# Performance work log

Measured on AMD Instinct MI355X. Metric: run time of the kernel, lower is better.

Reference implementation:

```python
import jax, jax.numpy as jnp
import numpy as np

COLOR_SIZE = 4
SIZE = 64
FILTERS = 512
LENGTH = SIZE * SIZE * 3  # 12288


def setup_inputs() -> dict:
    key = jax.random.key(0)
    k1, k2, k3 = jax.random.split(key, 3)
    example = jax.random.randint(k1, (8, SIZE, SIZE, 3), 0, COLOR_SIZE, dtype=jnp.int32)
    kernel = jax.random.normal(k2, (FILTERS, LENGTH), dtype=jnp.float32)
    bias = jnp.zeros((FILTERS,), dtype=jnp.float32)
    dense_w = jax.random.normal(k3, (FILTERS, COLOR_SIZE), dtype=jnp.float32) * 0.02
    dense_b = jnp.zeros((COLOR_SIZE,), dtype=jnp.float32)
    return {"example": example, "kernel": kernel, "bias": bias,
            "dense_w": dense_w, "dense_b": dense_b}


def reference(example, kernel, bias, dense_w, dense_b):
    B = example.shape[0]
    L = kernel.shape[1]  # 12288
    # normalize int pixels to [-1, 1)
    x = example.astype(jnp.float32) / COLOR_SIZE * 2.0 - 1.0
    x = x.reshape(B, L)                                   # [B, L]
    # FFT-based long (causal full) convolution, fft_length = 2L
    Xf = jnp.fft.rfft(x, n=2 * L, axis=-1)                # [B, L+1] complex64
    Kf = jnp.fft.rfft(kernel, n=2 * L, axis=-1)           # [F, L+1]
    y = jnp.fft.irfft(Xf[:, None, :] * Kf[None, :, :], n=2 * L, axis=-1)[..., :L]  # [B, F, L]
    y = jnp.transpose(y, (0, 2, 1)) + bias                # [B, L, F]
    y = jax.nn.relu(y)
    out = y @ dense_w + dense_b                           # [B, L, color_size]
    return out.reshape(B, SIZE, SIZE, 3, COLOR_SIZE).astype(jnp.float32)
```

## Files before the change

kernel.cpp:

```cpp
#include <hip/hip_runtime.h>

#define FF 512
#define LL 12288
#define NJC 1556
#define NR 128

typedef _Float16 half8 __attribute__((ext_vector_type(8)));
typedef float    f32x16 __attribute__((ext_vector_type(16)));

__global__ __launch_bounds__(256) void build_At(const float* __restrict__ kern,
                                                _Float16* __restrict__ At) {
    int tid  = blockIdx.x * 256 + threadIdx.x;
    int lane = tid & 63;
    int rest = tid >> 6;
    int kc   = rest % 768;
    int fgt  = rest / 768;
    int f    = fgt * 32 + (lane & 31);
    int d0   = kc * 16 + (lane >> 5) * 8;
    const float* src = kern + (size_t)f * LL + d0;
    half8 v;
#pragma unroll
    for (int i = 0; i < 8; ++i) v[i] = (_Float16)src[i];
    ((half8*)At)[tid] = v;
}

__global__ __launch_bounds__(256) void build_XB(const int* __restrict__ ex,
                                                _Float16* __restrict__ XB) {
    int tid = blockIdx.x * 256 + threadIdx.x;
    if (tid >= NJC * NR) return;
    int r  = tid & 127;
    int jc = tid >> 7;
    int s  = r >> 3, b = r & 7;
    int j0 = jc * 8;
    half8 v;
#pragma unroll
    for (int i = 0; i < 8; ++i) {
        int idx = LL - 1 - (j0 + i) - s;
        float x = 0.f;
        if (idx >= 0) x = (float)ex[b * LL + idx] * 0.5f - 1.0f;
        v[i] = (_Float16)x;
    }
    ((half8*)XB)[tid] = v;
}

__global__ __launch_bounds__(256) void init_out(const float* __restrict__ db,
                                                float* __restrict__ out) {
    int tid = blockIdx.x * 256 + threadIdx.x;
    out[tid] = db[tid & 3];
}

__device__ __forceinline__ void gl_lds16(const half8* g, half8* l) {
    __builtin_amdgcn_global_load_lds((const __attribute__((address_space(1))) void*)g,
                                     (__attribute__((address_space(3))) void*)l, 16, 0, 0);
}

__global__ __launch_bounds__(256, 2) void conv_main(const _Float16* __restrict__ At,
                                                    const _Float16* __restrict__ XB,
                                                    const float* __restrict__ bias,
                                                    const float* __restrict__ dw,
                                                    float* __restrict__ out) {
    __shared__ half8 Abuf[2][8][4][64];

    int bx    = blockIdx.x;
    int slot  = bx & 7;
    int f_blk = slot >> 1;
    int n_blk = 383 - ((bx >> 3) * 2 + (slot & 1));
    int n0 = n_blk << 5;
    int M  = (n_blk + 4) >> 2;

    int tid  = threadIdx.x;
    int lane = tid & 63;
    int wid  = tid >> 6;
    int bb   = lane & 7;
    int nq   = (lane >> 3) & 3;
    int kh   = lane >> 5;

    const half8* Ag = (const half8*)At;
    const half8* ag[8];
#pragma unroll
    for (int u = 0; u < 8; ++u) {
        int kcl = wid * 2 + (u >> 2);
        int ft  = u & 3;
        ag[u] = Ag + ((size_t)(f_blk * 4 + ft) * 768 + kcl) * 64 + lane;
    }

    const half8* Bg = (const half8*)XB;
    const half8* pB[2];
#pragma unroll
    for (int cf = 0; cf < 2; ++cf) {
        int n  = n0 + wid * 8 + cf * 4 + nq;
        int T  = LL - 1 - n + 8 * kh;
        pB[cf] = Bg + (size_t)(T >> 3) * 128 + (T & 7) * 8 + bb;
    }

    f32x16 acc[4][2];
#pragma unroll
    for (int rf = 0; rf < 4; ++rf)
#pragma unroll
        for (int cf = 0; cf < 2; ++cf)
#pragma unroll
            for (int i = 0; i < 16; ++i) acc[rf][cf][i] = 0.f;

#pragma unroll
    for (int u = 0; u < 8; ++u)
        gl_lds16(ag[u], &Abuf[0][wid * 2 + (u >> 2)][u & 3][lane]);
    half8 b0[2], b1[2], b2[2];
#pragma unroll
    for (int cf = 0; cf < 2; ++cf) {
        b0[cf] = pB[cf][0];
        b1[cf] = pB[cf][256];
        pB[cf] += 512;
    }
    __syncthreads();

    for (int mc = 0; mc < M; ++mc) {
        int buf = mc & 1;
        if (mc + 1 < M) {
            size_t oa = (size_t)(mc + 1) * 512;
#pragma unroll
            for (int u = 0; u < 8; ++u)
                gl_lds16(ag[u] + oa, &Abuf[buf ^ 1][wid * 2 + (u >> 2)][u & 3][lane]);
        }
#pragma unroll
        for (int kc = 0; kc < 8; ++kc) {
#pragma unroll
            for (int cf = 0; cf < 2; ++cf) { b2[cf] = pB[cf][0]; pB[cf] += 256; }
            half8 a[4];
#pragma unroll
            for (int rf = 0; rf < 4; ++rf) a[rf] = Abuf[buf][kc][rf][lane];
#pragma unroll
            for (int rf = 0; rf < 4; ++rf)
#pragma unroll
                for (int cf = 0; cf < 2; ++cf)
                    acc[rf][cf] = __builtin_amdgcn_mfma_f32_32x32x16_f16(a[rf], b0[cf], acc[rf][cf], 0, 0, 0);
#pragma unroll
            for (int cf = 0; cf < 2; ++cf) { b0[cf] = b1[cf]; b1[cf] = b2[cf]; }
        }
        __syncthreads();
    }

    float p[2][4];
#pragma unroll
    for (int cf = 0; cf < 2; ++cf)
#pragma unroll
        for (int c = 0; c < 4; ++c) p[cf][c] = 0.f;

#pragma unroll
    for (int rf = 0; rf < 4; ++rf) {
#pragma unroll
        for (int reg = 0; reg < 16; ++reg) {
            int f = f_blk * 128 + rf * 32 + (reg & 3) + 8 * (reg >> 2) + 4 * kh;
            float bs = bias[f];
            float4 w = *(const float4*)(dw + (size_t)f * 4);
#pragma unroll
            for (int cf = 0; cf < 2; ++cf) {
                float y = fmaxf(acc[rf][cf][reg] + bs, 0.f);
                p[cf][0] += y * w.x; p[cf][1] += y * w.y;
                p[cf][2] += y * w.z; p[cf][3] += y * w.w;
            }
        }
    }
#pragma unroll
    for (int cf = 0; cf < 2; ++cf)
#pragma unroll
        for (int c = 0; c < 4; ++c)
            p[cf][c] += __shfl_xor(p[cf][c], 32, 64);
    if (kh == 0) {
#pragma unroll
        for (int cf = 0; cf < 2; ++cf) {
            int n = n0 + wid * 8 + cf * 4 + nq;
            float* o = out + ((size_t)bb * LL + n) * 4;
#pragma unroll
            for (int c = 0; c < 4; ++c) atomicAdd(o + c, p[cf][c]);
        }
    }
}

extern "C" void kernel_launch(void* const* d_in, const int* in_sizes, int n_in,
                              void* d_out, int out_size, void* d_ws, size_t ws_size,
                              hipStream_t stream) {
    const int*   ex   = (const int*)d_in[0];
    const float* kern = (const float*)d_in[1];
    const float* bias = (const float*)d_in[2];
    const float* dw   = (const float*)d_in[3];
    const float* db   = (const float*)d_in[4];
    float* out = (float*)d_out;

    _Float16* At = (_Float16*)d_ws;
    _Float16* XB = (_Float16*)((char*)d_ws + (size_t)FF * LL * 2);

    hipLaunchKernelGGL(build_At, dim3(3072), dim3(256), 0, stream, kern, At);
    hipLaunchKernelGGL(build_XB, dim3(778),  dim3(256), 0, stream, ex, XB);
    hipLaunchKernelGGL(init_out, dim3(1536), dim3(256), 0, stream, db, out);
    hipLaunchKernelGGL(conv_main, dim3(1536), dim3(256), 0, stream, At, XB, bias, dw, out);
}
```

Measured before the change: 534.5 us.

## Replace syncthreads with vmcnt-limited barriers and deepen B-operand prefetch

Replaces each __syncthreads in the main GEMM loop with an explicit s_waitcnt vmcnt plus s_barrier. The wait drains only the older LDS-bound A loads and leaves the newer B register loads in flight across the barrier. The kc loop now processes two k-chunks per step, with B operands prefetched a full step ahead, and raises wave priority around the MFMA bursts. The guard on the next-chunk prefetch is removed, so the last iteration issues an extra A prefetch. For the final filter tile that prefetch reads past the At region into the adjacent workspace and writes into an unused LDS buffer. The hand-written wait counts rely on exact load ordering, which is fragile.

Measured after the change: 565.1 us. 5.7% more time.

```diff
diff --git a/kernel.cpp b/kernel.cpp
--- a/kernel.cpp
+++ b/kernel.cpp
@@ -104,39 +104,61 @@
 #pragma unroll
     for (int u = 0; u < 8; ++u)
         gl_lds16(ag[u], &Abuf[0][wid * 2 + (u >> 2)][u & 3][lane]);
-    half8 b0[2], b1[2], b2[2];
+    __builtin_amdgcn_sched_barrier(0);
+    half8 bc[2][2], bn[2][2];
 #pragma unroll
     for (int cf = 0; cf < 2; ++cf) {
-        b0[cf] = pB[cf][0];
-        b1[cf] = pB[cf][256];
+        bc[0][cf] = pB[cf][0];
+        bc[1][cf] = pB[cf][256];
         pB[cf] += 512;
     }
-    __syncthreads();
+    __builtin_amdgcn_sched_barrier(0);
+    asm volatile("s_waitcnt vmcnt(4)" ::: "memory");
+    __builtin_amdgcn_s_barrier();
+    __builtin_amdgcn_sched_barrier(0);
 
     for (int mc = 0; mc < M; ++mc) {
         int buf = mc & 1;
-        if (mc + 1 < M) {
-            size_t oa = (size_t)(mc + 1) * 512;
-#pragma unroll
-            for (int u = 0; u < 8; ++u)
-                gl_lds16(ag[u] + oa, &Abuf[buf ^ 1][wid * 2 + (u >> 2)][u & 3][lane]);
+        size_t oa = (size_t)(mc + 1) * 512;
+#pragma unroll
+        for (int u = 0; u < 8; ++u)
+            gl_lds16(ag[u] + oa, &Abuf[buf ^ 1][wid * 2 + (u >> 2)][u & 3][lane]);
+        __builtin_amdgcn_sched_barrier(0);
+
+#pragma unroll
+        for (int w = 0; w < 4; ++w) {
+#pragma unroll
+            for (int cf = 0; cf < 2; ++cf) {
+                bn[0][cf] = pB[cf][0];
+                bn[1][cf] = pB[cf][256];
+                pB[cf] += 512;
+            }
+            half8 a2[2][4];
+#pragma unroll
+            for (int h = 0; h < 2; ++h)
+#pragma unroll
+                for (int rf = 0; rf < 4; ++rf)
+                    a2[h][rf] = Abuf[buf][2 * w + h][rf][lane];
+            __builtin_amdgcn_s_setprio(1);
+#pragma unroll
+            for (int h = 0; h < 2; ++h)
+#pragma unroll
+                for (int rf = 0; rf < 4; ++rf)
+#pragma unroll
+                    for (int cf = 0; cf < 2; ++cf)
+                        acc[rf][cf] = __builtin_amdgcn_mfma_f32_32x32x16_f16(
+                            a2[h][rf], bc[h][cf], acc[rf][cf], 0, 0, 0);
+            __builtin_amdgcn_s_setprio(0);
+#pragma unroll
+            for (int h = 0; h < 2; ++h)
+#pragma unroll
+                for (int cf = 0; cf < 2; ++cf) bc[h][cf] = bn[h][cf];
         }
-#pragma unroll
-        for (int kc = 0; kc < 8; ++kc) {
-#pragma unroll
-            for (int cf = 0; cf < 2; ++cf) { b2[cf] = pB[cf][0]; pB[cf] += 256; }
-            half8 a[4];
-#pragma unroll
-            for (int rf = 0; rf < 4; ++rf) a[rf] = Abuf[buf][kc][rf][lane];
-#pragma unroll
-            for (int rf = 0; rf < 4; ++rf)
-#pragma unroll
-                for (int cf = 0; cf < 2; ++cf)
-                    acc[rf][cf] = __builtin_amdgcn_mfma_f32_32x32x16_f16(a[rf], b0[cf], acc[rf][cf], 0, 0, 0);
-#pragma unroll
-            for (int cf = 0; cf < 2; ++cf) { b0[cf] = b1[cf]; b1[cf] = b2[cf]; }
-        }
-        __syncthreads();
+
+        __builtin_amdgcn_sched_barrier(0);
+        asm volatile("s_waitcnt vmcnt(16)" ::: "memory");
+        __builtin_amdgcn_s_barrier();
+        __builtin_amdgcn_sched_barrier(0);
     }
 
     float p[2][4];
```
